# Kernel tuning notes

Hardware: AMD Instinct MI355X
Metric: run time of the kernel (lower is better)

## Reference

```python
import jax, jax.numpy as jnp
import numpy as np

NEG = -1e9

def _leaky(x, slope):
    return jnp.where(x >= 0, x, slope * x)

def _mlp_sig(x, w1, b1, w2, b2):
    # Linear -> LeakyReLU(0.01) -> Linear -> Sigmoid  (a graph_discover expert)
    return jax.nn.sigmoid(_leaky(x @ w1 + b1, 0.01) @ w2 + b2)

def _gatv2(x, adj, wl, bl, wr, br, we, att, bias):
    # Dense-masked GATv2Conv (PyG semantics): edge s->t exists iff adj[b,s,t] != 0,
    # edge_attr is the adjacency value (edge_dim=1), heads concatenated.
    B, Np, _ = x.shape
    heads, out_ch = att.shape
    xl = (x @ wl + bl).reshape(B, Np, heads, out_ch)  # source transform (messages)
    xr = (x @ wr + br).reshape(B, Np, heads, out_ch)  # target transform
    adjT = jnp.swapaxes(adj, 1, 2)                    # [b, target, source]
    ea = adjT[..., None, None] * we.reshape(heads, out_ch)   # lin_edge (no bias)
    e = _leaky(xl[:, None, :, :, :] + xr[:, :, None, :, :] + ea, 0.2)  # (B,T,S,H,O)
    logits = jnp.einsum('btsho,ho->btsh', e, att)
    m = adjT != 0
    logits = jnp.where(m[..., None], logits, NEG)
    alpha = jax.nn.softmax(logits, axis=2) * m[..., None]    # zero rows with no in-edges
    out = jnp.einsum('btsh,bsho->btho', alpha, xl)
    return out.reshape(B, Np, heads * out_ch) + bias

def _forward(latent, gumbel_noise,
             d0_w1, d0_b1, d0_w2, d0_b2,
             d1_w1, d1_b1, d1_w2, d1_b2,
             a_w, a_b,
             g1_wl, g1_bl, g1_wr, g1_br, g1_we, g1_att, g1_bias,
             g2_wl, g2_bl, g2_wr, g2_br, g2_we, g2_att, g2_bias):
    B, C, Hh, Ww = latent.shape
    N = Hh * Ww
    lat = jnp.transpose(latent, (0, 2, 3, 1)).reshape(B, N, C)
    # positional encoding (dropout = identity in eval)
    pos = jnp.arange(N, dtype=jnp.float32)[:, None]
    div = jnp.exp(jnp.arange(0, C, 2, dtype=jnp.float32) * (-np.log(10000.0) / C))
    pe = jnp.zeros((N, C), lat.dtype).at[:, 0::2].set(jnp.sin(pos * div)).at[:, 1::2].set(jnp.cos(pos * div))
    pl = lat + pe
    mask = jnp.zeros((B, N, 1), lat.dtype)  # forward() hardcodes mask = 0

    # pairwise node concat: inp[b, i*N+j] = [pl[b,i], pl[b,j]]
    ni = jnp.repeat(pl, N, axis=1)
    nj = jnp.tile(pl, (1, N, 1))
    inp = jnp.concatenate([ni, nj], axis=-1)  # (B, N*N, 2C)
    no_inter = _mlp_sig(inp, d0_w1, d0_b1, d0_w2, d0_b2).reshape(B, N, N)
    # action = zeros -> argmax = 0 for every row -> all rows routed to expert graph_discovers[1]
    inter = _mlp_sig(inp, d1_w1, d1_b1, d1_w2, d1_b2).reshape(B, N, N)
    adj = no_inter * (1 - mask) + inter * mask

    # differentiable Bernoulli via hard gumbel-softmax (straight-through)
    logits = jnp.log(jnp.clip(jnp.stack([1 - adj, adj], axis=-1), 1e-4))
    y = jax.nn.softmax(logits + gumbel_noise, axis=-1)
    y_hard = jax.nn.one_hot(jnp.argmax(y, axis=-1), 2, dtype=y.dtype)
    cg = (y_hard + y - jax.lax.stop_gradient(y))[..., 1]
    weighted = adj * cg

    # _compute_y, noise='off': append action node, pad adjacency (right col = 1, bottom row = 0)
    action = jnp.zeros((B, a_w.shape[0]), lat.dtype)
    action_node = action @ a_w + a_b
    nodes = jnp.concatenate([pl, action_node[:, None, :]], axis=1)  # (B, N+1, C)
    adj_p = jnp.pad(weighted, ((0, 0), (0, 0), (0, 1)), constant_values=1.0)
    adj_p = jnp.pad(adj_p, ((0, 0), (0, 1), (0, 0)), constant_values=0.0)

    x1 = _leaky(_gatv2(nodes, adj_p, g1_wl, g1_bl, g1_wr, g1_br, g1_we, g1_att, g1_bias), 0.01)
    x2 = _gatv2(x1, adj_p, g2_wl, g2_bl, g2_wr, g2_br, g2_we, g2_att, g2_bias)  # (B, N+1, heads*C)
    ny = x2[:, :N, :]
    # action argmax = 0 -> gathered head is columns [C, 2C)
    out = ny[..., :C] * (1 - mask) + ny[..., C:2 * C] * mask
    return jax.nn.softmax(out, axis=-1)

def setup_inputs() -> dict:
    key = jax.random.key(0)
    ks = jax.random.split(key, 32)
    B, C, Hh, Ww = 4, 64, 14, 14
    N = Hh * Ww
    A = 4
    heads = 1 + A
    D0, O1 = 800, 100
    f32 = jnp.float32
    def nrm(k, shp, sc=0.05):
        return jax.random.normal(k, shp, f32) * sc
    return {
        'latent': jax.random.normal(ks[0], (B, C, Hh, Ww), f32),
        'gumbel_noise': jax.random.gumbel(ks[1], (B, N, N, 2), f32),
        'd0_w1': nrm(ks[2], (2 * C, D0)), 'd0_b1': jnp.zeros((D0,), f32),
        'd0_w2': nrm(ks[3], (D0, 1)), 'd0_b2': jnp.zeros((1,), f32),
        'd1_w1': nrm(ks[4], (2 * C, D0)), 'd1_b1': jnp.zeros((D0,), f32),
        'd1_w2': nrm(ks[5], (D0, 1)), 'd1_b2': jnp.zeros((1,), f32),
        'a_w': nrm(ks[6], (A, C)), 'a_b': nrm(ks[7], (C,)),
        'g1_wl': nrm(ks[8], (C, heads * O1)), 'g1_bl': jnp.zeros((heads * O1,), f32),
        'g1_wr': nrm(ks[9], (C, heads * O1)), 'g1_br': jnp.zeros((heads * O1,), f32),
        'g1_we': nrm(ks[10], (heads * O1,)), 'g1_att': nrm(ks[11], (heads, O1)),
        'g1_bias': jnp.zeros((heads * O1,), f32),
        'g2_wl': nrm(ks[12], (heads * O1, heads * C)), 'g2_bl': jnp.zeros((heads * C,), f32),
        'g2_wr': nrm(ks[13], (heads * O1, heads * C)), 'g2_br': jnp.zeros((heads * C,), f32),
        'g2_we': nrm(ks[14], (heads * C,)), 'g2_att': nrm(ks[15], (heads, C)),
        'g2_bias': jnp.zeros((heads * C,), f32),
    }

def reference(latent, gumbel_noise,
              d0_w1, d0_b1, d0_w2, d0_b2,
              d1_w1, d1_b1, d1_w2, d1_b2,
              a_w, a_b,
              g1_wl, g1_bl, g1_wr, g1_br, g1_we, g1_att, g1_bias,
              g2_wl, g2_bl, g2_wr, g2_br, g2_we, g2_att, g2_bias):
    return _forward(latent, gumbel_noise,
                    d0_w1, d0_b1, d0_w2, d0_b2,
                    d1_w1, d1_b1, d1_w2, d1_b2,
                    a_w, a_b,
                    g1_wl, g1_bl, g1_wr, g1_br, g1_we, g1_att, g1_bias,
                    g2_wl, g2_bl, g2_wr, g2_br, g2_we, g2_att, g2_bias)
```

## Files before the change

kernel.cpp:

```cpp
#include <hip/hip_runtime.h>
#include <math.h>

#define NB 4
#define NN 196
#define NC 64
#define ND0 800
#define NH 5
#define NO1 100
#define NC1 500
#define NO2 64
#define TT 2
#define JC 4
#define JW 200
#define TQ 2
#define NEGF -1000000000.0f
#define TH_MARGIN 0.002f

__global__ void __launch_bounds__(256)
k_head(const float* __restrict__ latent,
       const float* __restrict__ w1, const float* __restrict__ b1,
       const float* __restrict__ wl, const float* __restrict__ bl,
       const float* __restrict__ wr, const float* __restrict__ br,
       double* __restrict__ U, double* __restrict__ V, float* __restrict__ VT_f,
       float* __restrict__ xl1, float* __restrict__ xl1T, float* __restrict__ xr1,
       int* __restrict__ bcount) {
    __shared__ double rowd[2][NC];
    __shared__ float  rowf[NC];
    int bi = blockIdx.x;
    int tid = threadIdx.x;
    if (bi == 0 && tid == 0) *bcount = 0;
    if (bi < NB*(NN/2)) {
        int b = bi / (NN/2);
        int n0 = (bi % (NN/2)) * 2;
        if (tid < 128) {
            int r = tid >> 6, c = tid & 63;
            int n = n0 + r;
            double div = exp((double)(2*(c >> 1)) * (-log(10000.0) / (double)NC));
            double ang = (double)n * div;
            double pe = (c & 1) ? cos(ang) : sin(ang);
            rowd[r][c] = (double)latent[(b*NC + c)*NN + n] + pe;
        }
        __syncthreads();
        size_t bn0 = (size_t)(b*NN + n0);
        for (int j = tid; j < ND0; j += 256) {
            double au0 = 0.0, au1 = 0.0;
            double av0 = (double)b1[j], av1 = av0;
            #pragma unroll 8
            for (int k = 0; k < NC; ++k) {
                double p0 = rowd[0][k], p1 = rowd[1][k];
                double wu = (double)w1[k*ND0 + j];
                double wv = (double)w1[(NC + k)*ND0 + j];
                au0 += p0 * wu; au1 += p1 * wu;
                av0 += p0 * wv; av1 += p1 * wv;
            }
            U[bn0*ND0 + j] = au0;
            U[(bn0 + 1)*ND0 + j] = au1;
            V[bn0*ND0 + j] = av0;
            V[(bn0 + 1)*ND0 + j] = av1;
            VT_f[((size_t)b*ND0 + j)*NN + n0] = (float)av0;
            VT_f[((size_t)b*ND0 + j)*NN + n0 + 1] = (float)av1;
        }
    } else {
        int bn = bi - NB*(NN/2);
        int b = bn / NN, n = bn % NN;
        if (tid < NC) {
            int c = tid;
            double div = exp((double)(2*(c >> 1)) * (-log(10000.0) / (double)NC));
            double ang = (double)n * div;
            double pe = (c & 1) ? cos(ang) : sin(ang);
            rowf[c] = (float)((double)latent[(b*NC + c)*NN + n] + pe);
        }
        __syncthreads();
        for (int c = tid; c < NC1; c += 256) {
            float al = bl[c], ar = br[c];
            #pragma unroll 8
            for (int k = 0; k < NC; ++k) {
                float p = rowf[k];
                al += p * wl[k*NC1 + c];
                ar += p * wr[k*NC1 + c];
            }
            xl1[(size_t)bn*NC1 + c] = al;
            xr1[(size_t)bn*NC1 + c] = ar;
            xl1T[((size_t)b*NC1 + c)*256 + n] = al;
        }
    }
}

__global__ void __launch_bounds__(1024)
k_adj32(const double* __restrict__ U, const float* __restrict__ VT,
        const float* __restrict__ w2, const float* __restrict__ b2,
        const float* __restrict__ gum, float* __restrict__ WT,
        int* __restrict__ blist, int* __restrict__ bcount) {
    __shared__ float Ul[TT][ND0];
    __shared__ float w2l[ND0];
    __shared__ float part[JC][TT][256];
    int bi = blockIdx.x;
    int b = bi / (NN/TT);
    int t0 = (bi % (NN/TT)) * TT;
    int tid = threadIdx.x;
    int s = tid & 255;
    int chunk = tid >> 8;
    for (int idx = tid; idx < TT*ND0; idx += 1024) {
        int tt = idx / ND0, j = idx - tt*ND0;
        Ul[tt][j] = (float)U[((size_t)(b*NN + t0 + tt))*ND0 + j];
    }
    for (int j = tid; j < ND0; j += 1024) w2l[j] = w2[j];
    __syncthreads();
    float a0 = 0.0f, a1 = 0.0f;
    if (s < NN) {
        const float* vp = VT + ((size_t)b*ND0 + chunk*JW)*NN + s;
        int j0 = chunk*JW;
        #pragma unroll 4
        for (int jj = 0; jj < JW; ++jj) {
            float v = vp[(size_t)jj*NN];
            float w = w2l[j0 + jj];
            float h0 = Ul[0][j0 + jj] + v; h0 = (h0 >= 0.0f) ? h0 : 0.01f*h0; a0 = fmaf(h0, w, a0);
            float h1 = Ul[1][j0 + jj] + v; h1 = (h1 >= 0.0f) ? h1 : 0.01f*h1; a1 = fmaf(h1, w, a1);
        }
    }
    part[chunk][0][s] = a0;
    part[chunk][1][s] = a1;
    __syncthreads();
    if (tid < TT*NN) {
        int tt = tid / NN, ss = tid - tt*NN;
        float acc = b2[0] + part[0][tt][ss] + part[1][tt][ss]
                  + part[2][tt][ss] + part[3][tt][ss];
        int t = t0 + tt;
        float adj = 1.0f/(1.0f + expf(-acc));
        float l1 = logf(fmaxf(adj, 1e-4f));
        float l0 = logf(fmaxf(1.0f - adj, 1e-4f));
        float g0 = gum[((size_t)(b*NN + t)*NN + ss)*2 + 0];
        float g1 = gum[((size_t)(b*NN + t)*NN + ss)*2 + 1];
        float margin = (l1 + g1) - (l0 + g0);
        if (fabsf(margin) <= TH_MARGIN) {
            int li = atomicAdd(bcount, 1);
            blist[li] = (b*NN + t)*NN + ss;
        }
        WT[((size_t)(b*NN + ss))*NN + t] = (margin > 0.0f) ? adj : 0.0f;
    }
}

__global__ void __launch_bounds__(256)
k_adjfix(const double* __restrict__ U, const double* __restrict__ V,
         const float* __restrict__ w2, const float* __restrict__ b2,
         const float* __restrict__ gum, const int* __restrict__ blist,
         const int* __restrict__ bcount, float* __restrict__ WT) {
    int nfix = *bcount;
    int gwid = (blockIdx.x * blockDim.x + threadIdx.x) >> 6;
    int lane = threadIdx.x & 63;
    int nw = (gridDim.x * blockDim.x) >> 6;
    for (int i = gwid; i < nfix; i += nw) {
        int code = blist[i];
        int s = code % NN;
        int t = (code / NN) % NN;
        int b = code / (NN*NN);
        const double* up = U + ((size_t)(b*NN + t))*ND0;
        const double* vp = V + ((size_t)(b*NN + s))*ND0;
        double a = 0.0;
        for (int j = lane; j < ND0; j += 64) {
            double h = up[j] + vp[j];
            h = (h >= 0.0) ? h : 0.01*h;
            a += h * (double)w2[j];
        }
        for (int off = 32; off >= 1; off >>= 1) a += __shfl_xor(a, off);
        if (lane == 0) {
            double acc = a + (double)b2[0];
            double adj = 1.0/(1.0 + exp(-acc));
            double l1 = log(fmax(adj, 1e-4));
            double l0 = log(fmax(1.0 - adj, 1e-4));
            double g0 = (double)gum[((size_t)(b*NN + t)*NN + s)*2 + 0];
            double g1 = (double)gum[((size_t)(b*NN + t)*NN + s)*2 + 1];
            double z0 = l0 + g0, z1 = l1 + g1;
            double m = fmax(z0, z1);
            double e0 = exp(z0 - m), e1 = exp(z1 - m);
            double sm = e0 + e1;
            int cg = (e1/sm) > (e0/sm);
            WT[((size_t)(b*NN + s))*NN + t] = cg ? (float)adj : 0.0f;
        }
    }
}

__global__ void __launch_bounds__(256)
k_gat1a(const float* __restrict__ xl1T, const float* __restrict__ xr1,
        const float* __restrict__ WT, const float* __restrict__ we,
        const float* __restrict__ att, float* __restrict__ alphaG) {
    __shared__ float wred[4];
    __shared__ float mxs, sms;
    int blk = blockIdx.x;
    int t = blk % NN;
    int bh = blk / NN;
    int h = bh % NH;
    int b = bh / NH;
    int s = threadIdx.x;
    int lane = s & 63, wid = s >> 6;
    float wt = (s < NN) ? WT[((size_t)(b*NN + t))*NN + s] : 0.0f;
    const float* xT  = xl1T + ((size_t)b*NC1 + h*NO1)*256;
    const float* xr  = xr1 + ((size_t)(b*NN + t))*NC1 + h*NO1;
    const float* weh = we + h*NO1;
    const float* ath = att + h*NO1;
    float a = 0.0f;
    #pragma unroll 5
    for (int o = 0; o < NO1; ++o) {
        float x = xT[(size_t)o*256 + s];
        float v = fmaf(wt, weh[o], x + xr[o]);
        float av = ath[o];
        a += fmaxf(v, 0.0f)*av + fminf(v, 0.0f)*(0.2f*av);
    }
    bool on = (s < NN) && (wt != 0.0f);
    float m = on ? a : NEGF;
    #pragma unroll
    for (int off = 32; off >= 1; off >>= 1) m = fmaxf(m, __shfl_xor(m, off));
    if (lane == 0) wred[wid] = m;
    __syncthreads();
    if (s == 0) mxs = fmaxf(fmaxf(wred[0], wred[1]), fmaxf(wred[2], wred[3]));
    __syncthreads();
    float e = on ? expf(a - mxs) : 0.0f;
    float r = e;
    #pragma unroll
    for (int off = 32; off >= 1; off >>= 1) r += __shfl_xor(r, off);
    if (lane == 0) wred[wid] = r;
    __syncthreads();
    if (s == 0) sms = wred[0] + wred[1] + wred[2] + wred[3];
    __syncthreads();
    alphaG[(size_t)blk*256 + s] = (sms > 0.0f) ? e / sms : 0.0f;
}

__global__ void __launch_bounds__(640)
k_gat1b(const float* __restrict__ xl1, const float* __restrict__ alphaG,
        const float* __restrict__ bias, float* __restrict__ x1) {
    int blk = blockIdx.x;
    int b = blk / (NN/TQ), tq = blk % (NN/TQ);
    int tid = threadIdx.x;
    int w = tid >> 6, l = tid & 63;
    int h = w >> 1, csub = w & 1;
    int o = csub*64 + l;
    bool active = (o < NO1);
    int c = h*NO1 + (active ? o : 0);
    const float* ap = alphaG + (((size_t)b*NH + h)*NN + tq*TQ)*256;
    const float* xp = xl1 + (size_t)b*NN*NC1 + c;
    float a0 = 0.f, a1 = 0.f;
    for (int s = 0; s < NN; ++s) {
        float x = xp[(size_t)s*NC1];
        a0 = fmaf(ap[s], x, a0);
        a1 = fmaf(ap[256 + s], x, a1);
    }
    if (active) {
        float bs = bias[c];
        float v;
        v = a0 + bs; x1[((size_t)(b*NN + tq*TQ + 0))*NC1 + c] = (v >= 0.f) ? v : 0.01f*v;
        v = a1 + bs; x1[((size_t)(b*NN + tq*TQ + 1))*NC1 + c] = (v >= 0.f) ? v : 0.01f*v;
    }
}

__global__ void k_proj2(const float* __restrict__ x1, const float* __restrict__ wl, const float* __restrict__ bl,
                        const float* __restrict__ wr, const float* __restrict__ br,
                        float* __restrict__ xl2, float* __restrict__ xl2T, float* __restrict__ xr2) {
    __shared__ float row[NC1];
    __shared__ float part[256];
    int bn = blockIdx.x;
    int b = bn / NN, n = bn % NN;
    int tid = threadIdx.x;
    for (int c = tid; c < NC1; c += 256) row[c] = x1[(size_t)bn*NC1 + c];
    __syncthreads();
    int which = tid >> 7;
    int o = tid & 63;
    int half = (tid >> 6) & 1;
    const float* w = which ? wr : wl;
    float acc = 0.0f;
    for (int k = half*250; k < half*250 + 250; ++k)
        acc += row[k] * w[(size_t)k*320 + o];
    part[tid] = acc;
    __syncthreads();
    if ((tid & 64) == 0) {
        float tot = part[tid] + part[tid + 64];
        if (which == 0) {
            float v = tot + bl[o];
            xl2[(size_t)bn*NO2 + o] = v;
            xl2T[((size_t)b*NO2 + o)*256 + n] = v;
        } else {
            xr2[(size_t)bn*NO2 + o] = tot + br[o];
        }
    }
}

__global__ void __launch_bounds__(256)
k_gat2(const float* __restrict__ xl2T, const float* __restrict__ xl2,
       const float* __restrict__ xr2, const float* __restrict__ WT,
       const float* __restrict__ we, const float* __restrict__ att,
       const float* __restrict__ bias, float* __restrict__ out) {
    __shared__ float red[256], alpha_l[256], part[4][NO2];
    __shared__ float mxs, sms;
    int blk = blockIdx.x;
    int b = blk / NN, t = blk % NN;
    int s = threadIdx.x;
    float wt = (s < NN) ? WT[((size_t)(b*NN + t))*NN + s] : 0.0f;
    const float* xT = xl2T + (size_t)b*NO2*256;
    const float* xr = xr2 + ((size_t)(b*NN + t))*NO2;
    float acc = 0.0f;
    for (int c = 0; c < NO2; ++c) {
        float x = xT[(size_t)c*256 + s];
        float v = fmaf(wt, we[c], x + xr[c]);
        float av = att[c];
        acc += fmaxf(v, 0.0f)*av + fminf(v, 0.0f)*(0.2f*av);
    }
    bool on = (s < NN) && (wt != 0.0f);
    float lgt = on ? acc : NEGF;
    red[s] = lgt;
    __syncthreads();
    for (int d = 128; d >= 1; d >>= 1) {
        if (s < d) red[s] = fmaxf(red[s], red[s + d]);
        __syncthreads();
    }
    if (s == 0) mxs = red[0];
    __syncthreads();
    float e = on ? expf(acc - mxs) : 0.0f;
    red[s] = e;
    __syncthreads();
    for (int d = 128; d >= 1; d >>= 1) {
        if (s < d) red[s] += red[s + d];
        __syncthreads();
    }
    if (s == 0) sms = red[0];
    __syncthreads();
    alpha_l[s] = (sms > 0.0f) ? e / sms : 0.0f;
    __syncthreads();
    int c = s & 63, sq = s >> 6;
    float pa = 0.0f;
    const float* xp = xl2 + (size_t)b*NN*NO2 + c;
    for (int ss = sq*49; ss < sq*49 + 49; ++ss)
        pa = fmaf(alpha_l[ss], xp[(size_t)ss*NO2], pa);
    part[sq][c] = pa;
    __syncthreads();
    if (s < NO2) {
        float ny = part[0][s] + part[1][s] + part[2][s] + part[3][s] + bias[s];
        float m = ny;
        for (int off = 32; off >= 1; off >>= 1) m = fmaxf(m, __shfl_xor(m, off));
        float ee = expf(ny - m);
        float ssum = ee;
        for (int off = 32; off >= 1; off >>= 1) ssum += __shfl_xor(ssum, off);
        out[((size_t)(b*NN + t))*NO2 + s] = ee / ssum;
    }
}

extern "C" void kernel_launch(void* const* d_in, const int* in_sizes, int n_in,
                              void* d_out, int out_size, void* d_ws, size_t ws_size,
                              hipStream_t stream) {
    const float* latent  = (const float*)d_in[0];
    const float* gum     = (const float*)d_in[1];
    const float* d0_w1   = (const float*)d_in[2];
    const float* d0_b1   = (const float*)d_in[3];
    const float* d0_w2   = (const float*)d_in[4];
    const float* d0_b2   = (const float*)d_in[5];
    const float* g1_wl   = (const float*)d_in[12];
    const float* g1_bl   = (const float*)d_in[13];
    const float* g1_wr   = (const float*)d_in[14];
    const float* g1_br   = (const float*)d_in[15];
    const float* g1_we   = (const float*)d_in[16];
    const float* g1_att  = (const float*)d_in[17];
    const float* g1_bias = (const float*)d_in[18];
    const float* g2_wl   = (const float*)d_in[19];
    const float* g2_bl   = (const float*)d_in[20];
    const float* g2_wr   = (const float*)d_in[21];
    const float* g2_br   = (const float*)d_in[22];
    const float* g2_we   = (const float*)d_in[23];
    const float* g2_att  = (const float*)d_in[24];
    const float* g2_bias = (const float*)d_in[25];
    float* out = (float*)d_out;

    char* ws = (char*)d_ws;
    size_t off = 0;
    auto alloc = [&](size_t bytes) { char* p = ws + off; off += (bytes + 255) & ~(size_t)255; return (void*)p; };
    double* U_d   = (double*)alloc((size_t)NB*NN*ND0*8);
    double* V_d   = (double*)alloc((size_t)NB*NN*ND0*8);
    float*  VT_f  = (float*) alloc((size_t)NB*ND0*NN*4);
    float*  WT    = (float*) alloc((size_t)NB*NN*NN*4);
    float*  xl1   = (float*) alloc((size_t)NB*NN*NC1*4);
    float*  xl1T  = (float*) alloc((size_t)NB*NC1*256*4);
    float*  xr1   = (float*) alloc((size_t)NB*NN*NC1*4);
    float*  alphaG= (float*) alloc((size_t)NB*NH*NN*256*4);
    float*  x1    = (float*) alloc((size_t)NB*NN*NC1*4);
    float*  xl2   = (float*) alloc((size_t)NB*NN*NO2*4);
    float*  xl2T  = (float*) alloc((size_t)NB*NO2*256*4);
    float*  xr2   = (float*) alloc((size_t)NB*NN*NO2*4);
    int*    blist = (int*)   alloc((size_t)NB*NN*NN*4);
    int*    bcount= (int*)   alloc(256);

    hipLaunchKernelGGL(k_head,   dim3(NB*(NN/2) + NB*NN), dim3(256), 0, stream,
                       latent, d0_w1, d0_b1, g1_wl, g1_bl, g1_wr, g1_br,
                       U_d, V_d, VT_f, xl1, xl1T, xr1, bcount);
    hipLaunchKernelGGL(k_adj32,  dim3(NB*(NN/TT)),  dim3(1024), 0, stream, U_d, VT_f, d0_w2, d0_b2, gum, WT, blist, bcount);
    hipLaunchKernelGGL(k_adjfix, dim3(256),         dim3(256),  0, stream, U_d, V_d, d0_w2, d0_b2, gum, blist, bcount, WT);
    hipLaunchKernelGGL(k_gat1a,  dim3(NB*NH*NN),    dim3(256),  0, stream, xl1T, xr1, WT, g1_we, g1_att, alphaG);
    hipLaunchKernelGGL(k_gat1b,  dim3(NB*(NN/TQ)),  dim3(640),  0, stream, xl1, alphaG, g1_bias, x1);
    hipLaunchKernelGGL(k_proj2,  dim3(NB*NN),       dim3(256),  0, stream, x1, g2_wl, g2_bl, g2_wr, g2_br, xl2, xl2T, xr2);
    hipLaunchKernelGGL(k_gat2,   dim3(NB*NN),       dim3(256),  0, stream, xl2T, xl2, xr2, WT, g2_we, g2_att, g2_bias, out);
}
```

Before: 159.5 us.

## Drop double-precision U/V buffers; recompute first layer in fixup from positional rows

The head kernel no longer writes the large double-precision U and V arrays. It stores U in float, keeps the transposed float V, and saves only the double positional-encoded rows. The fixup kernel, which handles near-threshold pairs, now recomputes the first-layer pre-activations in double from those rows and w1 instead of reading stored U/V. The head kernel's blocking also changes from two rows per block to one row split across four blocks, which gives more parallelism but reloads the weights more often. The aim is to cut global memory traffic. The fixup path now does more arithmetic per pair, which matters if many pairs fall inside the margin.

After: 228.8 us. 1.43x slower.

```diff
diff --git a/kernel.cpp b/kernel.cpp
--- a/kernel.cpp
+++ b/kernel.cpp
@@ -21,47 +21,42 @@
        const float* __restrict__ w1, const float* __restrict__ b1,
        const float* __restrict__ wl, const float* __restrict__ bl,
        const float* __restrict__ wr, const float* __restrict__ br,
-       double* __restrict__ U, double* __restrict__ V, float* __restrict__ VT_f,
+       double* __restrict__ pl_d, float* __restrict__ U_f, float* __restrict__ VT_f,
        float* __restrict__ xl1, float* __restrict__ xl1T, float* __restrict__ xr1,
        int* __restrict__ bcount) {
-    __shared__ double rowd[2][NC];
+    __shared__ double rowd[NC];
     __shared__ float  rowf[NC];
     int bi = blockIdx.x;
     int tid = threadIdx.x;
     if (bi == 0 && tid == 0) *bcount = 0;
-    if (bi < NB*(NN/2)) {
-        int b = bi / (NN/2);
-        int n0 = (bi % (NN/2)) * 2;
-        if (tid < 128) {
-            int r = tid >> 6, c = tid & 63;
-            int n = n0 + r;
+    if (bi < NB*NN*4) {
+        int bn = bi >> 2;
+        int q = bi & 3;
+        int b = bn / NN, n = bn % NN;
+        if (tid < NC) {
+            int c = tid;
             double div = exp((double)(2*(c >> 1)) * (-log(10000.0) / (double)NC));
             double ang = (double)n * div;
             double pe = (c & 1) ? cos(ang) : sin(ang);
-            rowd[r][c] = (double)latent[(b*NC + c)*NN + n] + pe;
+            double v = (double)latent[(b*NC + c)*NN + n] + pe;
+            rowd[c] = v;
+            if (q == 0) pl_d[(size_t)bn*NC + c] = v;
         }
         __syncthreads();
-        size_t bn0 = (size_t)(b*NN + n0);
-        for (int j = tid; j < ND0; j += 256) {
-            double au0 = 0.0, au1 = 0.0;
-            double av0 = (double)b1[j], av1 = av0;
+        int j = q*200 + tid;
+        if (tid < 200) {
+            double au = 0.0, av = (double)b1[j];
             #pragma unroll 8
             for (int k = 0; k < NC; ++k) {
-                double p0 = rowd[0][k], p1 = rowd[1][k];
-                double wu = (double)w1[k*ND0 + j];
-                double wv = (double)w1[(NC + k)*ND0 + j];
-                au0 += p0 * wu; au1 += p1 * wu;
-                av0 += p0 * wv; av1 += p1 * wv;
+                double p = rowd[k];
+                au += p * (double)w1[k*ND0 + j];
+                av += p * (double)w1[(NC + k)*ND0 + j];
             }
-            U[bn0*ND0 + j] = au0;
-            U[(bn0 + 1)*ND0 + j] = au1;
-            V[bn0*ND0 + j] = av0;
-            V[(bn0 + 1)*ND0 + j] = av1;
-            VT_f[((size_t)b*ND0 + j)*NN + n0] = (float)av0;
-            VT_f[((size_t)b*ND0 + j)*NN + n0 + 1] = (float)av1;
+            U_f[(size_t)bn*ND0 + j] = (float)au;
+            VT_f[((size_t)b*ND0 + j)*NN + n] = (float)av;
         }
     } else {
-        int bn = bi - NB*(NN/2);
+        int bn = bi - NB*NN*4;
         int b = bn / NN, n = bn % NN;
         if (tid < NC) {
             int c = tid;
@@ -87,7 +82,7 @@
 }
 
 __global__ void __launch_bounds__(1024)
-k_adj32(const double* __restrict__ U, const float* __restrict__ VT,
+k_adj32(const float* __restrict__ U_f, const float* __restrict__ VT,
         const float* __restrict__ w2, const float* __restrict__ b2,
         const float* __restrict__ gum, float* __restrict__ WT,
         int* __restrict__ blist, int* __restrict__ bcount) {
@@ -102,7 +97,7 @@
     int chunk = tid >> 8;
     for (int idx = tid; idx < TT*ND0; idx += 1024) {
         int tt = idx / ND0, j = idx - tt*ND0;
-        Ul[tt][j] = (float)U[((size_t)(b*NN + t0 + tt))*ND0 + j];
+        Ul[tt][j] = U_f[((size_t)(b*NN + t0 + tt))*ND0 + j];
     }
     for (int j = tid; j < ND0; j += 1024) w2l[j] = w2[j];
     __syncthreads();
@@ -141,7 +136,8 @@
 }
 
 __global__ void __launch_bounds__(256)
-k_adjfix(const double* __restrict__ U, const double* __restrict__ V,
+k_adjfix(const double* __restrict__ pl_d, const float* __restrict__ w1,
+         const float* __restrict__ b1,
          const float* __restrict__ w2, const float* __restrict__ b2,
          const float* __restrict__ gum, const int* __restrict__ blist,
          const int* __restrict__ bcount, float* __restrict__ WT) {
@@ -154,11 +150,17 @@
         int s = code % NN;
         int t = (code / NN) % NN;
         int b = code / (NN*NN);
-        const double* up = U + ((size_t)(b*NN + t))*ND0;
-        const double* vp = V + ((size_t)(b*NN + s))*ND0;
+        const double* pt = pl_d + ((size_t)(b*NN + t))*NC;
+        const double* ps = pl_d + ((size_t)(b*NN + s))*NC;
         double a = 0.0;
         for (int j = lane; j < ND0; j += 64) {
-            double h = up[j] + vp[j];
+            double u = 0.0, vv = (double)b1[j];
+            #pragma unroll 8
+            for (int k = 0; k < NC; ++k) {
+                u  += pt[k] * (double)w1[k*ND0 + j];
+                vv += ps[k] * (double)w1[(NC + k)*ND0 + j];
+            }
+            double h = u + vv;
             h = (h >= 0.0) ? h : 0.01*h;
             a += h * (double)w2[j];
         }
@@ -370,8 +372,8 @@
     char* ws = (char*)d_ws;
     size_t off = 0;
     auto alloc = [&](size_t bytes) { char* p = ws + off; off += (bytes + 255) & ~(size_t)255; return (void*)p; };
-    double* U_d   = (double*)alloc((size_t)NB*NN*ND0*8);
-    double* V_d   = (double*)alloc((size_t)NB*NN*ND0*8);
+    double* pl_d  = (double*)alloc((size_t)NB*NN*NC*8);
+    float*  U_f   = (float*) alloc((size_t)NB*NN*ND0*4);
     float*  VT_f  = (float*) alloc((size_t)NB*ND0*NN*4);
     float*  WT    = (float*) alloc((size_t)NB*NN*NN*4);
     float*  xl1   = (float*) alloc((size_t)NB*NN*NC1*4);
@@ -385,11 +387,11 @@
     int*    blist = (int*)   alloc((size_t)NB*NN*NN*4);
     int*    bcount= (int*)   alloc(256);
 
-    hipLaunchKernelGGL(k_head,   dim3(NB*(NN/2) + NB*NN), dim3(256), 0, stream,
+    hipLaunchKernelGGL(k_head,   dim3(NB*NN*4 + NB*NN), dim3(256), 0, stream,
                        latent, d0_w1, d0_b1, g1_wl, g1_bl, g1_wr, g1_br,
-                       U_d, V_d, VT_f, xl1, xl1T, xr1, bcount);
-    hipLaunchKernelGGL(k_adj32,  dim3(NB*(NN/TT)),  dim3(1024), 0, stream, U_d, VT_f, d0_w2, d0_b2, gum, WT, blist, bcount);
-    hipLaunchKernelGGL(k_adjfix, dim3(256),         dim3(256),  0, stream, U_d, V_d, d0_w2, d0_b2, gum, blist, bcount, WT);
+                       pl_d, U_f, VT_f, xl1, xl1T, xr1, bcount);
+    hipLaunchKernelGGL(k_adj32,  dim3(NB*(NN/TT)),  dim3(1024), 0, stream, U_f, VT_f, d0_w2, d0_b2, gum, WT, blist, bcount);
+    hipLaunchKernelGGL(k_adjfix, dim3(256),         dim3(256),  0, stream, pl_d, d0_w1, d0_b1, d0_w2, d0_b2, gum, blist, bcount, WT);
     hipLaunchKernelGGL(k_gat1a,  dim3(NB*NH*NN),    dim3(256),  0, stream, xl1T, xr1, WT, g1_we, g1_att, alphaG);
     hipLaunchKernelGGL(k_gat1b,  dim3(NB*(NN/TQ)),  dim3(640),  0, stream, xl1, alphaG, g1_bias, x1);
     hipLaunchKernelGGL(k_proj2,  dim3(NB*NN),       dim3(256),  0, stream, x1, g2_wl, g2_bl, g2_wr, g2_br, xl2, xl2T, xr2);
```
